# Performance work log

Hardware: AMD Instinct MI355X
Metric: run time of the kernel (lower is better)

The kernel has to match this reference:

```python
import jax, jax.numpy as jnp
import numpy as np

N, D, H, F = 50000, 128, 8, 512
HD = D // H
EPS_BN = 1e-5


def _batchnorm(x, gamma, beta):
    # BatchNorm1d in training mode: per-feature batch stats over node dim
    m = x.mean(axis=0)
    v = x.var(axis=0)
    return (x - m) * jax.lax.rsqrt(v + EPS_BN) * gamma + beta


def setup_inputs() -> dict:
    key = jax.random.key(0)
    ks = jax.random.split(key, 12)
    s = 0.05
    return {
        "src": jax.random.normal(ks[0], (N, D), jnp.float32),
        "edge_index": jax.random.randint(ks[1], (2, 800000), 0, N, jnp.int64),
        "q_w": jax.random.normal(ks[2], (D, D), jnp.float32) * s,
        "q_b": jnp.zeros((D,), jnp.float32),
        "k_w": jax.random.normal(ks[3], (D, D), jnp.float32) * s,
        "v_w": jax.random.normal(ks[4], (D, D), jnp.float32) * s,
        "out_w": jax.random.normal(ks[5], (D, D), jnp.float32) * s,
        "out_b": jnp.zeros((D,), jnp.float32),
        "g1": jnp.ones((D,), jnp.float32),
        "b1": jnp.zeros((D,), jnp.float32),
        "lin1_w": jax.random.normal(ks[6], (F, D), jnp.float32) * s,
        "lin1_b": jnp.zeros((F,), jnp.float32),
        "lin2_w": jax.random.normal(ks[7], (D, F), jnp.float32) * s,
        "lin2_b": jnp.zeros((D,), jnp.float32),
        "g2": jnp.ones((D,), jnp.float32),
        "b2": jnp.zeros((D,), jnp.float32),
    }


def reference(src, edge_index, q_w, q_b, k_w, v_w, out_w, out_b,
              g1, b1, lin1_w, lin1_b, lin2_w, lin2_b, g2, b2):
    n = src.shape[0]
    # add self loops, then attention edge index is (dst=edge[1], src=edge[0])
    loops = jnp.arange(n, dtype=edge_index.dtype)
    ei = jnp.concatenate([edge_index, jnp.stack([loops, loops])], axis=1)
    e_src, e_dst = ei[0], ei[1]  # message flows e_src -> e_dst; query index = e_dst

    scaling = float(HD) ** (-0.5)
    q = ((src @ q_w.T + q_b) * scaling).reshape(n, H, HD)
    k = (src @ k_w.T).reshape(n, H, HD)
    v = (src @ v_w.T).reshape(n, H, HD)

    # per-edge scores [E, H]
    w = jnp.einsum("ehd,ehd->eh", q[e_dst], k[e_src])
    # deterministic segment softmax over edges grouped by destination node
    mx = jax.ops.segment_max(w, e_dst, num_segments=n)
    ex = jnp.exp(w - mx[e_dst])
    den = jax.ops.segment_sum(ex, e_dst, num_segments=n)
    attn_w = ex / (den[e_dst] + 1e-16)  # [E, H]

    # weighted scatter-add aggregation -> [n, H, HD]
    msgs = attn_w[:, :, None] * v[e_src]
    agg = jax.ops.segment_sum(msgs, e_dst, num_segments=n)

    attn_out = agg.reshape(n, D) @ out_w.T + out_b
    x = _batchnorm(src + attn_out, g1, b1)

    ff = jax.nn.leaky_relu(x @ lin1_w.T + lin1_b, negative_slope=0.01)
    ff = ff @ lin2_w.T + lin2_b
    x = _batchnorm(x + ff, g2, b2)
    return x
```

## Files before the change

### kernel.cpp

```cpp
#include <hip/hip_runtime.h>
#include <math.h>

#define D 128
#define H 8
#define HD 16

typedef __attribute__((ext_vector_type(8))) short bf16x8;
typedef __attribute__((ext_vector_type(4))) float f32x4;

#define GLOBAL_AS __attribute__((address_space(1)))
#define LDS_AS    __attribute__((address_space(3)))

__device__ __forceinline__ ushort f2bf(float x) {
    union { float f; unsigned u; } v; v.f = x;
    unsigned r = v.u + 0x7fffu + ((v.u >> 16) & 1u);
    return (ushort)(r >> 16);
}
__device__ __forceinline__ float bflo(unsigned u) {
    union { unsigned u; float f; } x; x.u = u << 16; return x.f;
}
__device__ __forceinline__ float bfhi(unsigned u) {
    union { unsigned u; float f; } x; x.u = u & 0xffff0000u; return x.f;
}
__device__ __forceinline__ float bf2f(short s) {
    union { unsigned u; float f; } x; x.u = ((unsigned)(ushort)s) << 16; return x.f;
}

__device__ __forceinline__ float dot16(const float* qf, uint4 a, uint4 b) {
    float w;
    w  = qf[0]  * bflo(a.x) + qf[1]  * bfhi(a.x);
    w += qf[2]  * bflo(a.y) + qf[3]  * bfhi(a.y);
    w += qf[4]  * bflo(a.z) + qf[5]  * bfhi(a.z);
    w += qf[6]  * bflo(a.w) + qf[7]  * bfhi(a.w);
    w += qf[8]  * bflo(b.x) + qf[9]  * bfhi(b.x);
    w += qf[10] * bflo(b.y) + qf[11] * bfhi(b.y);
    w += qf[12] * bflo(b.z) + qf[13] * bfhi(b.z);
    w += qf[14] * bflo(b.w) + qf[15] * bfhi(b.w);
    return w;
}
__device__ __forceinline__ void acc16(float* num, float e, uint4 a, uint4 b) {
    num[0]  = fmaf(e, bflo(a.x), num[0]);  num[1]  = fmaf(e, bfhi(a.x), num[1]);
    num[2]  = fmaf(e, bflo(a.y), num[2]);  num[3]  = fmaf(e, bfhi(a.y), num[3]);
    num[4]  = fmaf(e, bflo(a.z), num[4]);  num[5]  = fmaf(e, bfhi(a.z), num[5]);
    num[6]  = fmaf(e, bflo(a.w), num[6]);  num[7]  = fmaf(e, bfhi(a.w), num[7]);
    num[8]  = fmaf(e, bflo(b.x), num[8]);  num[9]  = fmaf(e, bfhi(b.x), num[9]);
    num[10] = fmaf(e, bflo(b.y), num[10]); num[11] = fmaf(e, bfhi(b.y), num[11]);
    num[12] = fmaf(e, bflo(b.z), num[12]); num[13] = fmaf(e, bfhi(b.z), num[13]);
    num[14] = fmaf(e, bflo(b.w), num[14]); num[15] = fmaf(e, bfhi(b.w), num[15]);
}

template<int EPI, int M, int STATS>
__global__ __launch_bounds__(256)
void gemm_v7_kernel(const ushort* __restrict__ A,
                    const ushort* __restrict__ W,
                    const float* __restrict__ bias,
                    const float* __restrict__ extf,
                    ushort* __restrict__ outb,
                    float* __restrict__ stats,
                    int N)
{
    __shared__ ushort alds[2][32 * 128];

    const int lane = threadIdx.x & 63, wave = threadIdx.x >> 6;
    const int lr = lane & 15, lq = lane >> 4;
    const int colbase = blockIdx.y * 128 + wave * 32;

    bf16x8 bfr[2][4];
    {
        const ushort* wp = W + (size_t)(colbase + lr) * 128 + lq * 8;
        #pragma unroll
        for (int ct = 0; ct < 2; ++ct)
            #pragma unroll
            for (int t = 0; t < 4; ++t)
                bfr[ct][t] = *(const bf16x8*)(wp + (size_t)ct * 16 * 128 + t * 32);
    }
    float biasv[2];
    biasv[0] = bias[colbase + lr];
    biasv[1] = bias[colbase + 16 + lr];

    float ssum[2] = {0.f, 0.f}, ssq[2] = {0.f, 0.f};

    auto stage = [&](int rb, int b) {
        #pragma unroll
        for (int i = 0; i < 2; ++i) {
            int r = wave * 8 + i * 4 + (lane >> 4);
            int gr = min(rb + r, N - 1);
            int c = (lane & 15) ^ (r & 7);
            __builtin_amdgcn_global_load_lds(
                (const GLOBAL_AS void*)(A + (size_t)gr * 128 + c * 8),
                (LDS_AS void*)(&alds[b][(wave * 8 + i * 4) * 128]),
                16, 0, 0);
        }
    };

    const int stride = gridDim.x * 32;
    int r0 = blockIdx.x * 32;

    stage(r0, 0);
    __syncthreads();
    int cur = 0;

    while (true) {
        int rn = r0 + stride;
        if (rn < N) stage(rn, cur ^ 1);

        bf16x8 a[2][4];
        #pragma unroll
        for (int s = 0; s < 2; ++s) {
            const ushort* lp = &alds[cur][(s * 16 + lr) * 128];
            #pragma unroll
            for (int t = 0; t < 4; ++t)
                a[s][t] = *(const bf16x8*)(lp + ((t * 4 + lq) ^ (lr & 7)) * 8);
        }

        f32x4 acc[2][2] = {};
        #pragma unroll
        for (int t = 0; t < 4; ++t) {
            acc[0][0] = __builtin_amdgcn_mfma_f32_16x16x32_bf16(a[0][t], bfr[0][t], acc[0][0], 0, 0, 0);
            acc[1][0] = __builtin_amdgcn_mfma_f32_16x16x32_bf16(a[1][t], bfr[0][t], acc[1][0], 0, 0, 0);
            acc[0][1] = __builtin_amdgcn_mfma_f32_16x16x32_bf16(a[0][t], bfr[1][t], acc[0][1], 0, 0, 0);
            acc[1][1] = __builtin_amdgcn_mfma_f32_16x16x32_bf16(a[1][t], bfr[1][t], acc[1][1], 0, 0, 0);
        }

        #pragma unroll
        for (int ct = 0; ct < 2; ++ct) {
            int gcol = colbase + ct * 16 + lr;
            #pragma unroll
            for (int s = 0; s < 2; ++s) {
                #pragma unroll
                for (int r = 0; r < 4; ++r) {
                    int grow = r0 + s * 16 + lq * 4 + r;
                    if (grow >= N) continue;
                    size_t o = (size_t)grow * M + gcol;
                    float v = acc[s][ct][r] + biasv[ct];
                    if (EPI == 2)      v = v > 0.f ? v : 0.01f * v;
                    else if (EPI == 3) v += extf[o];
                    if (STATS) { ssum[ct] += v; ssq[ct] = fmaf(v, v, ssq[ct]); }
                    outb[o] = f2bf(v);
                }
            }
        }

        if (rn >= N) break;
        __syncthreads();
        cur ^= 1;
        r0 = rn;
    }

    if (STATS) {
        #pragma unroll
        for (int ct = 0; ct < 2; ++ct) {
            float a = ssum[ct], b = ssq[ct];
            a += __shfl_xor(a, 16, 64);  b += __shfl_xor(b, 16, 64);
            a += __shfl_xor(a, 32, 64);  b += __shfl_xor(b, 32, 64);
            if (lq == 0) {
                unsafeAtomicAdd(&stats[colbase + ct * 16 + lr], a);
                unsafeAtomicAdd(&stats[128 + colbase + ct * 16 + lr], b);
            }
        }
    }
}

__global__ __launch_bounds__(256)
void lin2_v6_kernel(const ushort* __restrict__ Ap,
                    const ushort* __restrict__ W,
                    const float* __restrict__ bias,
                    const ushort* __restrict__ extb,
                    const float* __restrict__ rawstats,
                    const float* __restrict__ gg,
                    const float* __restrict__ bb,
                    ushort* __restrict__ outb,
                    int N)
{
    constexpr int K = 512;
    __shared__ ushort alds[32 * K];

    const int lane = threadIdx.x & 63, wave = threadIdx.x >> 6;
    const int lr = lane & 15, lq = lane >> 4;
    const int row0 = blockIdx.x * 32;
    const int c0w  = wave * 32;

    #pragma unroll
    for (int i = 0; i < 8; ++i) {
        int r = wave * 8 + i;
        int gr = min(row0 + r, N - 1);
        const ushort* gsrc = Ap + (size_t)gr * K + (size_t)((lane ^ (r & 7)) * 8);
        __builtin_amdgcn_global_load_lds(
            (const GLOBAL_AS void*)gsrc,
            (LDS_AS void*)(alds + (size_t)r * K),
            16, 0, 0);
    }

    bf16x8 wA[8], wB[8];
    auto loadW = [&](int kc, bf16x8 (&wd)[8]) {
        const ushort* wp0 = W + (size_t)(c0w + lr) * K + kc * 128 + lq * 8;
        #pragma unroll
        for (int t = 0; t < 4; ++t) {
            wd[t]     = *(const bf16x8*)(wp0 + t * 32);
            wd[4 + t] = *(const bf16x8*)(wp0 + (size_t)16 * K + t * 32);
        }
    };
    loadW(0, wA);
    loadW(1, wB);

    __syncthreads();

    f32x4 acc[2][2] = {};
    bf16x8 a[2][4];
    auto ldsA = [&](int kc) {
        #pragma unroll
        for (int s = 0; s < 2; ++s) {
            const ushort* lp = alds + (size_t)(s * 16 + lr) * K;
            #pragma unroll
            for (int t = 0; t < 4; ++t)
                a[s][t] = *(const bf16x8*)(lp + (kc * 16 + ((t * 4 + lq) ^ (lr & 7))) * 8);
        }
    };
    auto mf = [&](bf16x8 (&wd)[8]) {
        #pragma unroll
        for (int t = 0; t < 4; ++t) {
            acc[0][0] = __builtin_amdgcn_mfma_f32_16x16x32_bf16(a[0][t], wd[t],     acc[0][0], 0, 0, 0);
            acc[1][0] = __builtin_amdgcn_mfma_f32_16x16x32_bf16(a[1][t], wd[t],     acc[1][0], 0, 0, 0);
            acc[0][1] = __builtin_amdgcn_mfma_f32_16x16x32_bf16(a[0][t], wd[4 + t], acc[0][1], 0, 0, 0);
            acc[1][1] = __builtin_amdgcn_mfma_f32_16x16x32_bf16(a[1][t], wd[4 + t], acc[1][1], 0, 0, 0);
        }
    };

    ldsA(0); mf(wA);
    loadW(2, wA);
    ldsA(1); mf(wB);
    loadW(3, wB);
    ldsA(2); mf(wA);
    ldsA(3); mf(wB);

    #pragma unroll
    for (int ct = 0; ct < 2; ++ct) {
        int col = c0w + ct * 16 + lr;
        float biasv = bias[col];
        float mean = rawstats[col] / (float)N;
        float var  = rawstats[128 + col] / (float)N - mean * mean;
        float scv = gg[col] * rsqrtf(var + 1e-5f);
        float shv = bb[col] - mean * scv;
        #pragma unroll
        for (int s = 0; s < 2; ++s) {
            #pragma unroll
            for (int r = 0; r < 4; ++r) {
                int grow = row0 + s * 16 + lq * 4 + r;
                if (grow >= N) continue;
                size_t o = (size_t)grow * 128 + col;
                float v = acc[s][ct][r] + biasv + fmaf(bf2f((short)extb[o]), scv, shv);
                outb[o] = f2bf(v);
            }
        }
    }
}

__global__ __launch_bounds__(256)
void convert_deg_kernel(const float* __restrict__ qw, const float* __restrict__ qb,
                        const float* __restrict__ kw, const float* __restrict__ vw,
                        const float* __restrict__ ow, const float* __restrict__ w1,
                        const float* __restrict__ w2,
                        ushort* __restrict__ wqkv, ushort* __restrict__ wout,
                        ushort* __restrict__ w1b, ushort* __restrict__ w2b,
                        float* __restrict__ bqkv,
                        const float* __restrict__ src, ushort* __restrict__ srcbf,
                        int nd8,
                        const int* __restrict__ ei, long long E0,
                        int* __restrict__ deg)
{
    long long i = (long long)blockIdx.x * 256 + threadIdx.x;
    if (i < E0) atomicAdd(&deg[ei[E0 + i]], 1);
    if (i < nd8) {
        const float4* sp = (const float4*)(src + i * 8);
        float4 f0 = sp[0], f1 = sp[1];
        ushort u[8];
        u[0]=f2bf(f0.x); u[1]=f2bf(f0.y); u[2]=f2bf(f0.z); u[3]=f2bf(f0.w);
        u[4]=f2bf(f1.x); u[5]=f2bf(f1.y); u[6]=f2bf(f1.z); u[7]=f2bf(f1.w);
        *(uint4*)(srcbf + i * 8) = *(uint4*)u;
    }
    if (i < 49152) {
        int row = (int)i >> 7;
        float v;
        if (row < 128)      v = 0.25f * qw[i];
        else if (row < 256) v = kw[i - 16384];
        else                v = vw[i - 32768];
        wqkv[i] = f2bf(v);
        return;
    }
    long long j = i - 49152;
    if (j < 16384) { wout[j] = f2bf(ow[j]); return; }
    j -= 16384;
    if (j < 65536) { w1b[j] = f2bf(w1[j]); return; }
    j -= 65536;
    if (j < 65536) { w2b[j] = f2bf(w2[j]); return; }
    j -= 65536;
    if (j < 384) bqkv[j] = (j < 128) ? 0.25f * qb[j] : 0.f;
}

__global__ __launch_bounds__(256)
void w1fold_kernel(const ushort* __restrict__ w1b, const float* __restrict__ lb1,
                   const float* __restrict__ rawstats,
                   const float* __restrict__ g1, const float* __restrict__ b1,
                   ushort* __restrict__ w1f, float* __restrict__ bias1f, int N)
{
    int f = blockIdx.x * 4 + (threadIdx.x >> 6);
    int lane = threadIdx.x & 63;
    int k0 = lane * 2;
    float m0 = rawstats[k0] / (float)N;
    float v0 = rawstats[128 + k0] / (float)N - m0 * m0;
    float sc0 = g1[k0] * rsqrtf(v0 + 1e-5f);
    float sh0 = b1[k0] - m0 * sc0;
    float m1 = rawstats[k0 + 1] / (float)N;
    float v1 = rawstats[128 + k0 + 1] / (float)N - m1 * m1;
    float sc1 = g1[k0 + 1] * rsqrtf(v1 + 1e-5f);
    float sh1 = b1[k0 + 1] - m1 * sc1;

    uint wp = *(const uint*)(w1b + (size_t)f * 128 + k0);
    float w0 = bflo(wp), w1v = bfhi(wp);
    uint o = (uint)f2bf(w0 * sc0) | ((uint)f2bf(w1v * sc1) << 16);
    *(uint*)(w1f + (size_t)f * 128 + k0) = o;

    float part = w0 * sh0 + w1v * sh1;
    #pragma unroll
    for (int m = 1; m < 64; m <<= 1) part += __shfl_xor(part, m, 64);
    if (lane == 0) bias1f[f] = lb1[f] + part;
}

__global__ __launch_bounds__(256)
void scan_block_sum(const int* __restrict__ deg, int n, int* __restrict__ bsum)
{
    __shared__ int sh[256];
    int i = blockIdx.x * 256 + threadIdx.x;
    sh[threadIdx.x] = (i < n) ? deg[i] : 0;
    __syncthreads();
    for (int ofs = 128; ofs > 0; ofs >>= 1) {
        if (threadIdx.x < ofs) sh[threadIdx.x] += sh[threadIdx.x + ofs];
        __syncthreads();
    }
    if (threadIdx.x == 0) bsum[blockIdx.x] = sh[0];
}

__global__ __launch_bounds__(256)
void scan_final(const int* __restrict__ deg, int n, const int* __restrict__ bsum,
                int nb, int* __restrict__ rowptr)
{
    __shared__ int sb[256];
    __shared__ int sh[256];
    int t = threadIdx.x;
    sb[t] = (t < nb) ? bsum[t] : 0;
    __syncthreads();
    for (int ofs = 1; ofs < 256; ofs <<= 1) {
        int v = (t >= ofs) ? sb[t - ofs] : 0;
        __syncthreads();
        sb[t] += v;
        __syncthreads();
    }
    int boff = (blockIdx.x == 0) ? 0 : sb[blockIdx.x - 1];

    int i = blockIdx.x * 256 + t;
    int v = (i < n) ? deg[i] : 0;
    sh[t] = v;
    __syncthreads();
    for (int ofs = 1; ofs < 256; ofs <<= 1) {
        int u = (t >= ofs) ? sh[t - ofs] : 0;
        __syncthreads();
        sh[t] += u;
        __syncthreads();
    }
    if (i < n) rowptr[i] = boff + sh[t] - v;
    if (i == n - 1) rowptr[n] = boff + sh[t];
}

__global__ __launch_bounds__(256)
void scatter_kernel(const int* __restrict__ ei, long long E0,
                    const int* __restrict__ rowptr, int* __restrict__ cnt,
                    int* __restrict__ col)
{
    long long e = (long long)blockIdx.x * 256 + threadIdx.x;
    if (e >= E0) return;
    int s = ei[e], d = ei[E0 + e];
    int pos = rowptr[d] + atomicAdd(&cnt[d], 1);
    col[pos] = s;
}

__global__ __launch_bounds__(256)
void gat_agg_kernel(const int* __restrict__ rowptr, const int* __restrict__ col,
                    const ushort* __restrict__ qkv, ushort* __restrict__ agg, int N)
{
    int node = blockIdx.x * 4 + (threadIdx.x >> 6);
    if (node >= N) return;
    int lane = threadIdx.x & 63;
    int es = lane >> 3, h = lane & 7;
    const uint4* Q = (const uint4*)qkv;

    const uint4* qp = Q + (size_t)node * 48 + h * 2;
    uint4 qa = qp[0], qb = qp[1];
    float qf[16];
    qf[0]=bflo(qa.x); qf[1]=bfhi(qa.x); qf[2]=bflo(qa.y); qf[3]=bfhi(qa.y);
    qf[4]=bflo(qa.z); qf[5]=bfhi(qa.z); qf[6]=bflo(qa.w); qf[7]=bfhi(qa.w);
    qf[8]=bflo(qb.x); qf[9]=bfhi(qb.x); qf[10]=bflo(qb.y); qf[11]=bfhi(qb.y);
    qf[12]=bflo(qb.z); qf[13]=bfhi(qb.z); qf[14]=bflo(qb.w); qf[15]=bfhi(qb.w);

    float num[16];
    #pragma unroll
    for (int i = 0; i < 16; i++) num[i] = 0.f;
    float den = 0.f;

    int beg = rowptr[node];
    int total = rowptr[node + 1] - beg + 1;

    int idx = es;
    if (idx < total) {
        int s0 = (idx == 0) ? node : col[beg + idx - 1];
        const uint4* rp0 = Q + (size_t)s0 * 48 + h * 2;
        uint4 ka = rp0[16], kb = rp0[17], va = rp0[32], vb = rp0[33];
        int idx1 = idx + 8;
        int s1 = (idx1 < total) ? col[beg + idx1 - 1] : 0;

        while (true) {
            bool more = idx1 < total;
            uint4 ka1, kb1, va1, vb1;
            if (more) {
                const uint4* rp1 = Q + (size_t)s1 * 48 + h * 2;
                ka1 = rp1[16]; kb1 = rp1[17]; va1 = rp1[32]; vb1 = rp1[33];
            }
            int idx2 = idx1 + 8;
            int s2 = (idx2 < total) ? col[beg + idx2 - 1] : 0;

            float ev = __expf(dot16(qf, ka, kb));
            den += ev;
            acc16(num, ev, va, vb);

            if (!more) break;
            ka = ka1; kb = kb1; va = va1; vb = vb1;
            s1 = s2; idx1 = idx2;
        }
    }

    #pragma unroll
    for (int m = 8; m < 64; m <<= 1) {
        den += __shfl_xor(den, m, 64);
        #pragma unroll
        for (int i = 0; i < 16; i++) num[i] += __shfl_xor(num[i], m, 64);
    }

    if (es == 0) {
        float inv = 1.f / (den + 1e-16f);
        uint4 o0, o1;
        o0.x = (uint)f2bf(num[0]*inv)  | ((uint)f2bf(num[1]*inv)  << 16);
        o0.y = (uint)f2bf(num[2]*inv)  | ((uint)f2bf(num[3]*inv)  << 16);
        o0.z = (uint)f2bf(num[4]*inv)  | ((uint)f2bf(num[5]*inv)  << 16);
        o0.w = (uint)f2bf(num[6]*inv)  | ((uint)f2bf(num[7]*inv)  << 16);
        o1.x = (uint)f2bf(num[8]*inv)  | ((uint)f2bf(num[9]*inv)  << 16);
        o1.y = (uint)f2bf(num[10]*inv) | ((uint)f2bf(num[11]*inv) << 16);
        o1.z = (uint)f2bf(num[12]*inv) | ((uint)f2bf(num[13]*inv) << 16);
        o1.w = (uint)f2bf(num[14]*inv) | ((uint)f2bf(num[15]*inv) << 16);
        uint4* op = (uint4*)(agg + (size_t)node * 128 + h * 16);
        op[0] = o0; op[1] = o1;
    }
}

__global__ __launch_bounds__(256)
void bn_stats_bf16_kernel(const ushort* __restrict__ y, int N, float* __restrict__ stats)
{
    int jp = threadIdx.x & 63;
    int q4 = threadIdx.x >> 6;
    int r = blockIdx.x * 256 + q4;
    int rend = min(N, (int)(blockIdx.x + 1) * 256);
    float s0 = 0.f, qq0 = 0.f, s1 = 0.f, qq1 = 0.f;
    const uint* yp = (const uint*)y;
    for (; r < rend; r += 4) {
        uint u = yp[(size_t)r * 64 + jp];
        float a = bflo(u), b = bfhi(u);
        s0 += a; qq0 += a * a; s1 += b; qq1 += b * b;
    }
    __shared__ float sh[4][64][4];
    sh[q4][jp][0] = s0; sh[q4][jp][1] = qq0; sh[q4][jp][2] = s1; sh[q4][jp][3] = qq1;
    __syncthreads();
    if (threadIdx.x < 128) {
        int p = threadIdx.x >> 1;
        int w = threadIdx.x & 1;
        float ss = 0.f, sq = 0.f;
        #pragma unroll
        for (int i = 0; i < 4; i++) { ss += sh[i][p][w * 2]; sq += sh[i][p][w * 2 + 1]; }
        unsafeAtomicAdd(&stats[2 * p + w], ss);
        unsafeAtomicAdd(&stats[128 + 2 * p + w], sq);
    }
}

__global__ __launch_bounds__(256)
void bn_apply_out_kernel(const ushort* __restrict__ y, const float* __restrict__ rawstats,
                         const float* __restrict__ g, const float* __restrict__ b,
                         float* __restrict__ out, int total4, int N)
{
    __shared__ float scs[128], shs[128];
    if (threadIdx.x < 128) {
        int j = threadIdx.x;
        float mean = rawstats[j] / (float)N;
        float var  = rawstats[128 + j] / (float)N - mean * mean;
        float sc = g[j] * rsqrtf(var + 1e-5f);
        scs[j] = sc;
        shs[j] = b[j] - mean * sc;
    }
    __syncthreads();
    int i = blockIdx.x * 256 + threadIdx.x;
    if (i >= total4) return;
    uint2 u = reinterpret_cast<const uint2*>(y)[i];
    int j = (i * 4) & (D - 1);
    float4 v;
    v.x = bflo(u.x) * scs[j + 0] + shs[j + 0];
    v.y = bfhi(u.x) * scs[j + 1] + shs[j + 1];
    v.z = bflo(u.y) * scs[j + 2] + shs[j + 2];
    v.w = bfhi(u.y) * scs[j + 3] + shs[j + 3];
    reinterpret_cast<float4*>(out)[i] = v;
}

extern "C" void kernel_launch(void* const* d_in, const int* in_sizes, int n_in,
                              void* d_out, int out_size, void* d_ws, size_t ws_size,
                              hipStream_t stream)
{
    const float* src    = (const float*)d_in[0];
    const int*   ei     = (const int*)  d_in[1];
    const float* q_w    = (const float*)d_in[2];
    const float* q_b    = (const float*)d_in[3];
    const float* k_w    = (const float*)d_in[4];
    const float* v_w    = (const float*)d_in[5];
    const float* out_w  = (const float*)d_in[6];
    const float* out_b  = (const float*)d_in[7];
    const float* g1     = (const float*)d_in[8];
    const float* b1     = (const float*)d_in[9];
    const float* lin1_w = (const float*)d_in[10];
    const float* lin1_b = (const float*)d_in[11];
    const float* lin2_w = (const float*)d_in[12];
    const float* lin2_b = (const float*)d_in[13];
    const float* g2     = (const float*)d_in[14];
    const float* b2     = (const float*)d_in[15];

    const int N        = in_sizes[0] / D;
    const long long E0 = in_sizes[1] / 2;

    float* ws = (float*)d_ws;
    size_t off = 0;
    ushort* qkv   = (ushort*)(ws + off); off += (size_t)N * 192;
    ushort* agg   = (ushort*)(ws + off); off += (size_t)N * 64;
    ushort* srcbf = (ushort*)(ws + off); off += (size_t)N * 64;
    ushort* y1b   = (ushort*)(ws + off); off += (size_t)N * 64;
    ushort* hid   = (ushort*)(ws + off); off += (size_t)N * 256;
    ushort* y2b   = (ushort*)(ws + off); off += (size_t)N * 64;
    ushort* wqkv  = (ushort*)(ws + off); off += 24576;
    ushort* woutb = (ushort*)(ws + off); off += 8192;
    ushort* w1b   = (ushort*)(ws + off); off += 32768;
    ushort* w1f   = (ushort*)(ws + off); off += 32768;
    ushort* w2b   = (ushort*)(ws + off); off += 32768;
    float*  bqkv  = ws + off;            off += 384;
    float*  bias1f= ws + off;            off += 512;
    size_t zero_start = off;
    int* deg    = (int*)(ws + off); off += N;
    int* cnt    = (int*)(ws + off); off += N;
    float* stats1 = ws + off; off += 512;
    float* stats2 = ws + off; off += 512;
    size_t zero_cnt = off - zero_start;
    int* rowptr = (int*)(ws + off); off += N + 1;
    int* bsum   = (int*)(ws + off); off += 256;
    int* col    = (int*)(ws + off); off += E0;

    hipMemsetAsync(ws + zero_start, 0, zero_cnt * sizeof(float), stream);

    dim3 blk(256);

    dim3 gE0((unsigned)((E0 + 255) / 256));
    hipLaunchKernelGGL(convert_deg_kernel, gE0, blk, 0, stream,
                       q_w, q_b, k_w, v_w, out_w, lin1_w, lin2_w,
                       wqkv, woutb, w1b, w2b, bqkv,
                       src, srcbf, N * 16, ei, E0, deg);

    int nb = (N + 255) / 256;
    hipLaunchKernelGGL(scan_block_sum, dim3(nb), blk, 0, stream, deg, N, bsum);
    hipLaunchKernelGGL(scan_final, dim3(nb), blk, 0, stream, deg, N, bsum, nb, rowptr);
    hipLaunchKernelGGL(scatter_kernel, gE0, blk, 0, stream, ei, E0, rowptr, cnt, col);

    const int gx = 1024;

    hipLaunchKernelGGL((gemm_v7_kernel<0, 384, 0>), dim3(gx, 3), blk, 0, stream,
                       srcbf, wqkv, bqkv, nullptr, qkv, nullptr, N);

    hipLaunchKernelGGL(gat_agg_kernel, dim3((N + 3) / 4), blk, 0, stream,
                       rowptr, col, qkv, agg, N);

    hipLaunchKernelGGL((gemm_v7_kernel<3, 128, 1>), dim3(gx, 1), blk, 0, stream,
                       agg, woutb, out_b, src, y1b, stats1, N);

    hipLaunchKernelGGL(w1fold_kernel, dim3(128), blk, 0, stream,
                       w1b, lin1_b, stats1, g1, b1, w1f, bias1f, N);

    hipLaunchKernelGGL((gemm_v7_kernel<2, 512, 0>), dim3(gx, 4), blk, 0, stream,
                       y1b, w1f, bias1f, nullptr, hid, nullptr, N);

    hipLaunchKernelGGL(lin2_v6_kernel, dim3((N + 31) / 32), blk, 0, stream,
                       hid, w2b, lin2_b, y1b, stats1, g1, b1, y2b, N);

    dim3 gS((N + 255) / 256);
    hipLaunchKernelGGL(bn_stats_bf16_kernel, gS, blk, 0, stream, y2b, N, stats2);
    int total4 = N * D / 4;
    hipLaunchKernelGGL(bn_apply_out_kernel, dim3((total4 + 255) / 256), blk, 0, stream,
                       y2b, stats2, g2, b2, (float*)d_out, total4, N);
}
```

Before: 391.6 us.

## Transpose MFMA operands for vectorized epilogue stores and fuse BN2 stats into lin2

Swaps the MFMA A/B operands so each lane holds four consecutive output columns of one row. This lets the epilogues use 8-byte bf16 stores and float4 bias and residual loads in place of scattered 2-byte accesses. The lin2 kernel now also accumulates per-column sum and sum-of-squares for the second batchnorm and adds them atomically, which removes the separate bn_stats pass that re-read y2b. The cost is more shuffle reductions and twice as many atomics per block, and the stats are computed from fp32 values instead of the bf16-rounded ones.

```diff
diff --git a/kernel.cpp b/kernel.cpp
--- a/kernel.cpp
+++ b/kernel.cpp
@@ -51,7 +51,7 @@
 
 template<int EPI, int M, int STATS>
 __global__ __launch_bounds__(256)
-void gemm_v7_kernel(const ushort* __restrict__ A,
+void gemm_v8_kernel(const ushort* __restrict__ A,
                     const ushort* __restrict__ W,
                     const float* __restrict__ bias,
                     const float* __restrict__ extf,
@@ -74,11 +74,11 @@
             for (int t = 0; t < 4; ++t)
                 bfr[ct][t] = *(const bf16x8*)(wp + (size_t)ct * 16 * 128 + t * 32);
     }
-    float biasv[2];
-    biasv[0] = bias[colbase + lr];
-    biasv[1] = bias[colbase + 16 + lr];
-
-    float ssum[2] = {0.f, 0.f}, ssq[2] = {0.f, 0.f};
+    float4 biasv[2];
+    biasv[0] = *(const float4*)&bias[colbase + lq * 4];
+    biasv[1] = *(const float4*)&bias[colbase + 16 + lq * 4];
+
+    float ssum[2][4] = {}, ssq[2][4] = {};
 
     auto stage = [&](int rb, int b) {
         #pragma unroll
@@ -116,28 +116,42 @@
         f32x4 acc[2][2] = {};
         #pragma unroll
         for (int t = 0; t < 4; ++t) {
-            acc[0][0] = __builtin_amdgcn_mfma_f32_16x16x32_bf16(a[0][t], bfr[0][t], acc[0][0], 0, 0, 0);
-            acc[1][0] = __builtin_amdgcn_mfma_f32_16x16x32_bf16(a[1][t], bfr[0][t], acc[1][0], 0, 0, 0);
-            acc[0][1] = __builtin_amdgcn_mfma_f32_16x16x32_bf16(a[0][t], bfr[1][t], acc[0][1], 0, 0, 0);
-            acc[1][1] = __builtin_amdgcn_mfma_f32_16x16x32_bf16(a[1][t], bfr[1][t], acc[1][1], 0, 0, 0);
+            acc[0][0] = __builtin_amdgcn_mfma_f32_16x16x32_bf16(bfr[0][t], a[0][t], acc[0][0], 0, 0, 0);
+            acc[1][0] = __builtin_amdgcn_mfma_f32_16x16x32_bf16(bfr[0][t], a[1][t], acc[1][0], 0, 0, 0);
+            acc[0][1] = __builtin_amdgcn_mfma_f32_16x16x32_bf16(bfr[1][t], a[0][t], acc[0][1], 0, 0, 0);
+            acc[1][1] = __builtin_amdgcn_mfma_f32_16x16x32_bf16(bfr[1][t], a[1][t], acc[1][1], 0, 0, 0);
         }
 
         #pragma unroll
         for (int ct = 0; ct < 2; ++ct) {
-            int gcol = colbase + ct * 16 + lr;
+            int cb = colbase + ct * 16 + lq * 4;
             #pragma unroll
             for (int s = 0; s < 2; ++s) {
-                #pragma unroll
-                for (int r = 0; r < 4; ++r) {
-                    int grow = r0 + s * 16 + lq * 4 + r;
-                    if (grow >= N) continue;
-                    size_t o = (size_t)grow * M + gcol;
-                    float v = acc[s][ct][r] + biasv[ct];
-                    if (EPI == 2)      v = v > 0.f ? v : 0.01f * v;
-                    else if (EPI == 3) v += extf[o];
-                    if (STATS) { ssum[ct] += v; ssq[ct] = fmaf(v, v, ssq[ct]); }
-                    outb[o] = f2bf(v);
+                int grow = r0 + s * 16 + lr;
+                if (grow >= N) continue;
+                size_t o = (size_t)grow * M + cb;
+                float v0 = acc[s][ct][0] + biasv[ct].x;
+                float v1 = acc[s][ct][1] + biasv[ct].y;
+                float v2 = acc[s][ct][2] + biasv[ct].z;
+                float v3 = acc[s][ct][3] + biasv[ct].w;
+                if (EPI == 2) {
+                    v0 = v0 > 0.f ? v0 : 0.01f * v0;
+                    v1 = v1 > 0.f ? v1 : 0.01f * v1;
+                    v2 = v2 > 0.f ? v2 : 0.01f * v2;
+                    v3 = v3 > 0.f ? v3 : 0.01f * v3;
+                } else if (EPI == 3) {
+                    float4 e = *(const float4*)(extf + o);
+                    v0 += e.x; v1 += e.y; v2 += e.z; v3 += e.w;
                 }
+                if (STATS) {
+                    ssum[ct][0] += v0; ssq[ct][0] = fmaf(v0, v0, ssq[ct][0]);
+                    ssum[ct][1] += v1; ssq[ct][1] = fmaf(v1, v1, ssq[ct][1]);
+                    ssum[ct][2] += v2; ssq[ct][2] = fmaf(v2, v2, ssq[ct][2]);
+                    ssum[ct][3] += v3; ssq[ct][3] = fmaf(v3, v3, ssq[ct][3]);
+                }
+                ushort4 st;
+                st.x = f2bf(v0); st.y = f2bf(v1); st.z = f2bf(v2); st.w = f2bf(v3);
+                *(ushort4*)(outb + o) = st;
             }
         }
 
@@ -150,19 +164,25 @@
     if (STATS) {
         #pragma unroll
         for (int ct = 0; ct < 2; ++ct) {
-            float a = ssum[ct], b = ssq[ct];
-            a += __shfl_xor(a, 16, 64);  b += __shfl_xor(b, 16, 64);
-            a += __shfl_xor(a, 32, 64);  b += __shfl_xor(b, 32, 64);
-            if (lq == 0) {
-                unsafeAtomicAdd(&stats[colbase + ct * 16 + lr], a);
-                unsafeAtomicAdd(&stats[128 + colbase + ct * 16 + lr], b);
+            #pragma unroll
+            for (int i = 0; i < 4; ++i) {
+                float a = ssum[ct][i], b = ssq[ct][i];
+                a += __shfl_xor(a, 1, 64);  b += __shfl_xor(b, 1, 64);
+                a += __shfl_xor(a, 2, 64);  b += __shfl_xor(b, 2, 64);
+                a += __shfl_xor(a, 4, 64);  b += __shfl_xor(b, 4, 64);
+                a += __shfl_xor(a, 8, 64);  b += __shfl_xor(b, 8, 64);
+                if (lr == 0) {
+                    int col = colbase + ct * 16 + lq * 4 + i;
+                    unsafeAtomicAdd(&stats[col], a);
+                    unsafeAtomicAdd(&stats[128 + col], b);
+                }
             }
         }
     }
 }
 
 __global__ __launch_bounds__(256)
-void lin2_v6_kernel(const ushort* __restrict__ Ap,
+void lin2_v7_kernel(const ushort* __restrict__ Ap,
                     const ushort* __restrict__ W,
                     const float* __restrict__ bias,
                     const ushort* __restrict__ extb,
@@ -170,6 +190,7 @@
                     const float* __restrict__ gg,
                     const float* __restrict__ bb,
                     ushort* __restrict__ outb,
+                    float* __restrict__ stats2,
                     int N)
 {
     constexpr int K = 512;
@@ -219,10 +240,10 @@
     auto mf = [&](bf16x8 (&wd)[8]) {
         #pragma unroll
         for (int t = 0; t < 4; ++t) {
-            acc[0][0] = __builtin_amdgcn_mfma_f32_16x16x32_bf16(a[0][t], wd[t],     acc[0][0], 0, 0, 0);
-            acc[1][0] = __builtin_amdgcn_mfma_f32_16x16x32_bf16(a[1][t], wd[t],     acc[1][0], 0, 0, 0);
-            acc[0][1] = __builtin_amdgcn_mfma_f32_16x16x32_bf16(a[0][t], wd[4 + t], acc[0][1], 0, 0, 0);
-            acc[1][1] = __builtin_amdgcn_mfma_f32_16x16x32_bf16(a[1][t], wd[4 + t], acc[1][1], 0, 0, 0);
+            acc[0][0] = __builtin_amdgcn_mfma_f32_16x16x32_bf16(wd[t],     a[0][t], acc[0][0], 0, 0, 0);
+            acc[1][0] = __builtin_amdgcn_mfma_f32_16x16x32_bf16(wd[t],     a[1][t], acc[1][0], 0, 0, 0);
+            acc[0][1] = __builtin_amdgcn_mfma_f32_16x16x32_bf16(wd[4 + t], a[0][t], acc[0][1], 0, 0, 0);
+            acc[1][1] = __builtin_amdgcn_mfma_f32_16x16x32_bf16(wd[4 + t], a[1][t], acc[1][1], 0, 0, 0);
         }
     };
 
@@ -233,23 +254,62 @@
     ldsA(2); mf(wA);
     ldsA(3); mf(wB);
 
+    float ssum[2][4] = {}, ssq[2][4] = {};
+
     #pragma unroll
     for (int ct = 0; ct < 2; ++ct) {
-        int col = c0w + ct * 16 + lr;
-        float biasv = bias[col];
-        float mean = rawstats[col] / (float)N;
-        float var  = rawstats[128 + col] / (float)N - mean * mean;
-        float scv = gg[col] * rsqrtf(var + 1e-5f);
-        float shv = bb[col] - mean * scv;
+        int cb = c0w + ct * 16 + lq * 4;
+        float4 rs = *(const float4*)&rawstats[cb];
+        float4 rq = *(const float4*)&rawstats[128 + cb];
+        float4 g4 = *(const float4*)&gg[cb];
+        float4 b4 = *(const float4*)&bb[cb];
+        float4 bi = *(const float4*)&bias[cb];
+        float sc[4], ad[4];
+        {
+            float m0 = rs.x / (float)N, m1 = rs.y / (float)N,
+                  m2 = rs.z / (float)N, m3 = rs.w / (float)N;
+            sc[0] = g4.x * rsqrtf(rq.x / (float)N - m0 * m0 + 1e-5f);
+            sc[1] = g4.y * rsqrtf(rq.y / (float)N - m1 * m1 + 1e-5f);
+            sc[2] = g4.z * rsqrtf(rq.z / (float)N - m2 * m2 + 1e-5f);
+            sc[3] = g4.w * rsqrtf(rq.w / (float)N - m3 * m3 + 1e-5f);
+            ad[0] = bi.x + b4.x - m0 * sc[0];
+            ad[1] = bi.y + b4.y - m1 * sc[1];
+            ad[2] = bi.z + b4.z - m2 * sc[2];
+            ad[3] = bi.w + b4.w - m3 * sc[3];
+        }
         #pragma unroll
         for (int s = 0; s < 2; ++s) {
-            #pragma unroll
-            for (int r = 0; r < 4; ++r) {
-                int grow = row0 + s * 16 + lq * 4 + r;
-                if (grow >= N) continue;
-                size_t o = (size_t)grow * 128 + col;
-                float v = acc[s][ct][r] + biasv + fmaf(bf2f((short)extb[o]), scv, shv);
-                outb[o] = f2bf(v);
+            int grow = row0 + s * 16 + lr;
+            if (grow >= N) continue;
+            size_t o = (size_t)grow * 128 + cb;
+            ushort4 rv = *(const ushort4*)(extb + o);
+            float v0 = acc[s][ct][0] + ad[0] + bf2f((short)rv.x) * sc[0];
+            float v1 = acc[s][ct][1] + ad[1] + bf2f((short)rv.y) * sc[1];
+            float v2 = acc[s][ct][2] + ad[2] + bf2f((short)rv.z) * sc[2];
+            float v3 = acc[s][ct][3] + ad[3] + bf2f((short)rv.w) * sc[3];
+            ssum[ct][0] += v0; ssq[ct][0] = fmaf(v0, v0, ssq[ct][0]);
+            ssum[ct][1] += v1; ssq[ct][1] = fmaf(v1, v1, ssq[ct][1]);
+            ssum[ct][2] += v2; ssq[ct][2] = fmaf(v2, v2, ssq[ct][2]);
+            ssum[ct][3] += v3; ssq[ct][3] = fmaf(v3, v3, ssq[ct][3]);
+            ushort4 st;
+            st.x = f2bf(v0); st.y = f2bf(v1); st.z = f2bf(v2); st.w = f2bf(v3);
+            *(ushort4*)(outb + o) = st;
+        }
+    }
+
+    #pragma unroll
+    for (int ct = 0; ct < 2; ++ct) {
+        #pragma unroll
+        for (int i = 0; i < 4; ++i) {
+            float a = ssum[ct][i], b = ssq[ct][i];
+            a += __shfl_xor(a, 1, 64);  b += __shfl_xor(b, 1, 64);
+            a += __shfl_xor(a, 2, 64);  b += __shfl_xor(b, 2, 64);
+            a += __shfl_xor(a, 4, 64);  b += __shfl_xor(b, 4, 64);
+            a += __shfl_xor(a, 8, 64);  b += __shfl_xor(b, 8, 64);
+            if (lr == 0) {
+                int col = c0w + ct * 16 + lq * 4 + i;
+                unsafeAtomicAdd(&stats2[col], a);
+                unsafeAtomicAdd(&stats2[128 + col], b);
             }
         }
     }
@@ -457,34 +517,6 @@
         o1.w = (uint)f2bf(num[14]*inv) | ((uint)f2bf(num[15]*inv) << 16);
         uint4* op = (uint4*)(agg + (size_t)node * 128 + h * 16);
         op[0] = o0; op[1] = o1;
-    }
-}
-
-__global__ __launch_bounds__(256)
-void bn_stats_bf16_kernel(const ushort* __restrict__ y, int N, float* __restrict__ stats)
-{
-    int jp = threadIdx.x & 63;
-    int q4 = threadIdx.x >> 6;
-    int r = blockIdx.x * 256 + q4;
-    int rend = min(N, (int)(blockIdx.x + 1) * 256);
-    float s0 = 0.f, qq0 = 0.f, s1 = 0.f, qq1 = 0.f;
-    const uint* yp = (const uint*)y;
-    for (; r < rend; r += 4) {
-        uint u = yp[(size_t)r * 64 + jp];
-        float a = bflo(u), b = bfhi(u);
-        s0 += a; qq0 += a * a; s1 += b; qq1 += b * b;
-    }
-    __shared__ float sh[4][64][4];
-    sh[q4][jp][0] = s0; sh[q4][jp][1] = qq0; sh[q4][jp][2] = s1; sh[q4][jp][3] = qq1;
-    __syncthreads();
-    if (threadIdx.x < 128) {
-        int p = threadIdx.x >> 1;
-        int w = threadIdx.x & 1;
-        float ss = 0.f, sq = 0.f;
-        #pragma unroll
-        for (int i = 0; i < 4; i++) { ss += sh[i][p][w * 2]; sq += sh[i][p][w * 2 + 1]; }
-        unsafeAtomicAdd(&stats[2 * p + w], ss);
-        unsafeAtomicAdd(&stats[128 + 2 * p + w], sq);
     }
 }
 
@@ -581,26 +613,24 @@
 
     const int gx = 1024;
 
-    hipLaunchKernelGGL((gemm_v7_kernel<0, 384, 0>), dim3(gx, 3), blk, 0, stream,
+    hipLaunchKernelGGL((gemm_v8_kernel<0, 384, 0>), dim3(gx, 3), blk, 0, stream,
                        srcbf, wqkv, bqkv, nullptr, qkv, nullptr, N);
 
     hipLaunchKernelGGL(gat_agg_kernel, dim3((N + 3) / 4), blk, 0, stream,
                        rowptr, col, qkv, agg, N);
 
-    hipLaunchKernelGGL((gemm_v7_kernel<3, 128, 1>), dim3(gx, 1), blk, 0, stream,
+    hipLaunchKernelGGL((gemm_v8_kernel<3, 128, 1>), dim3(gx, 1), blk, 0, stream,
                        agg, woutb, out_b, src, y1b, stats1, N);
 
     hipLaunchKernelGGL(w1fold_kernel, dim3(128), blk, 0, stream,
                        w1b, lin1_b, stats1, g1, b1, w1f, bias1f, N);
 
-    hipLaunchKernelGGL((gemm_v7_kernel<2, 512, 0>), dim3(gx, 4), blk, 0, stream,
+    hipLaunchKernelGGL((gemm_v8_kernel<2, 512, 0>), dim3(gx, 4), blk, 0, stream,
                        y1b, w1f, bias1f, nullptr, hid, nullptr, N);
 
-    hipLaunchKernelGGL(lin2_v6_kernel, dim3((N + 31) / 32), blk, 0, stream,
-                       hid, w2b, lin2_b, y1b, stats1, g1, b1, y2b, N);
-
-    dim3 gS((N + 255) / 256);
-    hipLaunchKernelGGL(bn_stats_bf16_kernel, gS, blk, 0, stream, y2b, N, stats2);
+    hipLaunchKernelGGL(lin2_v7_kernel, dim3((N + 31) / 32), blk, 0, stream,
+                       hid, w2b, lin2_b, y1b, stats1, g1, b1, y2b, stats2, N);
+
     int total4 = N * D / 4;
     hipLaunchKernelGGL(bn_apply_out_kernel, dim3((total4 + 255) / 256), blk, 0, stream,
                        y2b, stats2, g2, b2, (float*)d_out, total4, N);
```

Result: slower. 584.8 us (+49.3%).
